# Optimization experiments

Measured on AMD Instinct MI355X. Metric: run time of the kernel, lower is better.

The kernel has to match this reference:

```python
import jax, jax.numpy as jnp
import numpy as np

B, HT_, WT_, DM, C = 32, 32, 32, 768, 64  # batch, token grid, token dim, hough channels
THETA_RES, RHO_RES = 3, 1


def hough_transform(rows, cols, theta_res, rho_res):
    """Precompute binary vote matrix [rows*cols, n_rho*n_theta] (HT-LCNN style)."""
    theta = np.linspace(0.0, 180.0, int(np.ceil(180.0 / theta_res)) + 1)[:-1]
    w = theta.size                                # n_theta
    diag = np.sqrt((rows - 1) ** 2 + (cols - 1) ** 2)
    q = int(np.ceil(diag / rho_res))
    nrho = 2 * q + 1                              # n_rho
    cos_t, sin_t = np.cos(np.deg2rad(theta)), np.sin(np.deg2rad(theta))
    ii, jj = np.meshgrid(np.arange(rows), np.arange(cols), indexing='ij')
    xc = jj - cols / 2.0                          # centered pixel coords
    yc = rows / 2.0 - ii
    rho = xc[..., None] * cos_t + yc[..., None] * sin_t   # [rows, cols, w]
    ridx = np.round(rho / rho_res).astype(np.int64) + q
    tidx = np.broadcast_to(np.arange(w), ridx.shape)
    flat = (ridx * w + tidx).reshape(rows * cols, w)      # bin = rho_idx*w + theta_idx
    vote = np.zeros((rows * cols, nrho * w), dtype=np.float32)
    vote[np.arange(rows * cols)[:, None], flat] = 1.0
    return vote, nrho, w


def setup_inputs() -> dict:
    key = jax.random.key(0)
    ks = jax.random.split(key, 8)
    vote_np, n_rho, n_theta = hough_transform(HT_, WT_, THETA_RES, RHO_RES)
    ch = C // 2
    s = lambda n: 1.0 / np.sqrt(n)
    return dict(
        tokens=jax.random.normal(ks[0], (B, HT_ * WT_, DM), jnp.float32),
        vote=jnp.asarray(vote_np),                                    # [N, HR]
        Wt_in=jax.random.normal(ks[1], (C, DM), jnp.float32) * s(DM),   # to_feats 1x1
        bt_in=jnp.zeros((C,), jnp.float32),
        W1=jax.random.normal(ks[2], (ch, C), jnp.float32) * s(C),       # conv1 1x1 (no bias)
        W2=jax.random.normal(ks[3], (ch, ch, 9, 1), jnp.float32) * s(ch * 9),  # (9,1) conv on hough map
        W3=jax.random.normal(ks[4], (C, ch), jnp.float32) * s(ch),      # conv3 1x1 (no bias)
        Wt_out=jax.random.normal(ks[5], (DM, C), jnp.float32) * s(C),   # from_feats 1x1
        bt_out=jnp.zeros((DM,), jnp.float32),
        n_rho=n_rho,
        n_theta=n_theta,
    )


def reference(tokens, vote, Wt_in, bt_in, W1, W2, W3, Wt_out, bt_out, n_rho, n_theta):
    # tokens: [B, N, D]; vote: [N, HR] with HR = n_rho * n_theta.
    # 1x1 convs over the token grid are position-independent -> plain matmuls on [B, N, *].
    norm = jnp.clip(vote.sum(0), 1.0)                       # [HR] HT vote-count normalizer
    feat = tokens @ Wt_in.T + bt_in                         # [B, N, C]   (to_feats)
    y = jax.nn.relu(feat @ W1.T)                            # [B, N, ch]  (conv1 + relu)
    # HT: relu (idempotent here) + vote gather as dense matmul, normalized per hough bin
    ht = jnp.einsum('bnc,nh->bch', y, vote) / norm          # [B, ch, HR]
    bb, ch, hr = ht.shape
    ht = ht.reshape(bb, ch, n_rho, n_theta)                 # [B, ch, n_rho, n_theta]
    ht = jax.lax.conv_general_dilated(                      # (9,1) conv along rho, pad 4
        ht, W2, (1, 1), ((4, 4), (0, 0)),
        dimension_numbers=('NCHW', 'OIHW', 'NCHW'))
    # IHT: relu + transposed vote scatter, normalized by n_theta
    iht = jnp.einsum('bch,nh->bnc', jax.nn.relu(ht.reshape(bb, ch, hr)), vote) / n_theta
    z = iht @ W3.T                                          # [B, N, C]   (conv3)
    out = (feat + z) @ Wt_out.T + bt_out                    # residual + from_feats -> [B, N, D]
    return out
```

## Files before the change

### kernel.cpp

```cpp
#include <hip/hip_runtime.h>
#include <math.h>

#define NB    32
#define NTOK  1024
#define DMODEL 768
#define CF    64
#define CHH   32
#define NRHO  89
#define NTH   60
#define HRB   (NRHO*NTH)

typedef short bf16x8 __attribute__((ext_vector_type(8)));
typedef float f32x4  __attribute__((ext_vector_type(4)));
typedef unsigned int uint;
typedef unsigned short ushort;
typedef unsigned char uchar;

__device__ __forceinline__ ushort f2bf(float f) {
    uint u = __float_as_uint(f);
    return (ushort)((u + 0x7FFF + ((u >> 16) & 1)) >> 16);
}
__device__ __forceinline__ float bf2f(ushort u) {
    return __uint_as_float(((uint)u) << 16);
}
__device__ __forceinline__ uint cvtpk(float lo, float hi) {
    uint r;
    asm("v_cvt_pk_bf16_f32 %0, %1, %2" : "=v"(r) : "v"(lo), "v"(hi));
    return r;
}

#define GLDS16(gp, lp) __builtin_amdgcn_global_load_lds( \
    (const __attribute__((address_space(1))) unsigned int*)(gp), \
    (__attribute__((address_space(3))) unsigned int*)(lp), 16, 0, 0)

__global__ __launch_bounds__(256) void k0_prep(
    int* __restrict__ perm, int* __restrict__ rowptr, uchar* __restrict__ rho8,
    const float* __restrict__ Wt_in, const float* __restrict__ bt_in,
    const float* __restrict__ W1, short* __restrict__ wcat,
    float* __restrict__ bcat,
    const float* __restrict__ Wt_out, const float* __restrict__ W2,
    short* __restrict__ wout, short* __restrict__ w2t) {
    __shared__ int rho_n[NTOK];
    __shared__ int cnt2[64 * 90];
    __shared__ int tot[96];
    __shared__ int base[96];
    __shared__ float w1row[64];
    const int tid = threadIdx.x;
    const int blk = blockIdx.x;

    if (blk < 60) {
        const int t = blk;
        const double rad = ((double)(t * 3)) * (M_PI / 180.0);
        const double ct = cos(rad), st = sin(rad);
        for (int n = tid; n < NTOK; n += 256) {
            int i = n >> 5, j = n & 31;
            double rho = (double)(j - 16) * ct + (double)(16 - i) * st;
            int ridx = (int)rint(rho) + 44;
            rho_n[n] = ridx;
            rho8[t * NTOK + n] = (uchar)ridx;
        }
        for (int i = tid; i < 64 * 90; i += 256) cnt2[i] = 0;
        __syncthreads();
        for (int n = tid; n < NTOK; n += 256)
            atomicAdd(&cnt2[(n >> 4) * 90 + rho_n[n]], 1);
        __syncthreads();
        if (tid < NRHO) {
            int s = 0;
            for (int c = 0; c < 64; ++c) {
                int v = cnt2[c * 90 + tid];
                cnt2[c * 90 + tid] = s;
                s += v;
            }
            tot[tid] = s;
        }
        __syncthreads();
        if (tid == 0) {
            int s = 0;
            for (int r = 0; r < NRHO; ++r) { base[r] = s; s += tot[r]; }
            base[NRHO] = s;
        }
        __syncthreads();
        if (tid < NRHO + 1) rowptr[t * 90 + tid] = base[tid];
        if (tid < 64) {
            const int c = tid;
            #pragma unroll
            for (int j = 0; j < 16; ++j) {
                int n = c * 16 + j;
                int r = rho_n[n];
                int cur = cnt2[c * 90 + r];
                cnt2[c * 90 + r] = cur + 1;
                perm[t * NTOK + base[r] + cur] = n;
            }
        }
    } else if (blk < 156) {
        const int c = blk - 60;
        if (c >= 64)
            for (int j = tid; j < 64; j += 256) w1row[j] = W1[(c - 64) * 64 + j];
        __syncthreads();
        for (int k = tid; k < DMODEL; k += 256) {
            float v;
            if (c < 64) v = Wt_in[c * DMODEL + k];
            else {
                v = 0.0f;
                for (int j = 0; j < 64; ++j) v += w1row[j] * Wt_in[j * DMODEL + k];
            }
            int kt = k >> 6, kk = k & 63;
            wcat[(((kt << 3) + (kk >> 3)) * 96 + c) * 8 + (k & 7)] = (short)f2bf(v);
        }
        if (tid == 0) {
            float bv;
            if (c < 64) bv = bt_in[c];
            else {
                bv = 0.0f;
                for (int j = 0; j < 64; ++j) bv += W1[(c - 64) * 64 + j] * bt_in[j];
            }
            bcat[c] = bv;
        }
    } else {
        int idx = (blk - 156) * 256 + tid;
        if (idx < 6144) {
            int d = idx >> 3, kg = idx & 7;
            float4 a = *(const float4*)&Wt_out[d * 64 + kg * 8];
            float4 b = *(const float4*)&Wt_out[d * 64 + kg * 8 + 4];
            uint4 v = make_uint4(cvtpk(a.x, a.y), cvtpk(a.z, a.w),
                                 cvtpk(b.x, b.y), cvtpk(b.z, b.w));
            *(uint4*)&wout[(((d >> 7) * 8 + kg) * 128 + (d & 127)) * 8] = v;
        } else if (idx < 6144 + 9216) {
            int q = idx - 6144;
            int e = q & 7, ln = (q >> 3) & 63, wm = (q >> 9) & 1, k = q >> 10;
            int o = wm * 16 + (ln & 15), i = ((ln >> 4) << 3) + e;
            w2t[q] = (short)f2bf(W2[(o * 32 + i) * 9 + k]);
        }
    }
}

__global__ __launch_bounds__(256) void k1_mfma(
    const float* __restrict__ tokens, const short* __restrict__ wcat,
    const float* __restrict__ bcat, ushort* __restrict__ featb,
    ushort* __restrict__ ybb) {
    __shared__ __align__(16) short Asm[2][4096];
    __shared__ __align__(16) short Bsm[2][6144];

    const int tid = threadIdx.x;
    const int lane = tid & 63, wave = tid >> 6;
    const int wm = wave >> 1, wn = wave & 1;
    const int row0 = blockIdx.x * 64;
    const int sm = tid >> 2, sq = tid & 3;

    const float* arow = tokens + (size_t)(row0 + sm) * DMODEL;

    f32x4 acc[2][3] = {};
    float4 ta[4];

    #pragma unroll
    for (int p = 0; p < 4; ++p)
        ta[p] = *(const float4*)&arow[(sq + 4 * p) * 4];
    for (int ch = tid; ch < 768; ch += 256)
        GLDS16((const char*)wcat + ch * 16, (char*)Bsm[0] + ch * 16);
    #pragma unroll
    for (int p = 0; p < 4; ++p) {
        int q = sq + 4 * p, kg = q >> 1, half = q & 1;
        uint lo = cvtpk(ta[p].x, ta[p].y);
        uint hi = cvtpk(ta[p].z, ta[p].w);
        *(uint2*)((char*)Asm[0] + (kg * 64 + sm) * 16 + half * 8) = make_uint2(lo, hi);
    }
    __syncthreads();

    int cur = 0;
    for (int kt = 0; kt < 12; ++kt) {
        if (kt < 11) {
            const float* src = arow + (kt + 1) * 64;
            #pragma unroll
            for (int p = 0; p < 4; ++p)
                ta[p] = *(const float4*)&src[(sq + 4 * p) * 4];
            const char* bsrc = (const char*)wcat + (size_t)(kt + 1) * 12288;
            for (int ch = tid; ch < 768; ch += 256)
                GLDS16(bsrc + ch * 16, (char*)Bsm[cur ^ 1] + ch * 16);
        }
        const bf16x8* Ap = (const bf16x8*)Asm[cur];
        const bf16x8* Bp = (const bf16x8*)Bsm[cur];
        #pragma unroll
        for (int ks = 0; ks < 2; ++ks) {
            int kg = (lane >> 4) + ks * 4;
            bf16x8 av[2], bv[3];
            #pragma unroll
            for (int i = 0; i < 2; ++i)
                av[i] = Ap[kg * 64 + wm * 32 + i * 16 + (lane & 15)];
            #pragma unroll
            for (int j = 0; j < 3; ++j)
                bv[j] = Bp[kg * 96 + wn * 48 + j * 16 + (lane & 15)];
            #pragma unroll
            for (int i = 0; i < 2; ++i)
                #pragma unroll
                for (int j = 0; j < 3; ++j)
                    acc[i][j] = __builtin_amdgcn_mfma_f32_16x16x32_bf16(
                        av[i], bv[j], acc[i][j], 0, 0, 0);
        }
        if (kt < 11) {
            #pragma unroll
            for (int p = 0; p < 4; ++p) {
                int q = sq + 4 * p, kg = q >> 1, half = q & 1;
                uint lo = cvtpk(ta[p].x, ta[p].y);
                uint hi = cvtpk(ta[p].z, ta[p].w);
                *(uint2*)((char*)Asm[cur ^ 1] + (kg * 64 + sm) * 16 + half * 8) =
                    make_uint2(lo, hi);
            }
        }
        __syncthreads();
        cur ^= 1;
    }

    ushort* fs = (ushort*)Asm[0];
    ushort* ys = (ushort*)Asm[1];
    float bb[3];
    #pragma unroll
    for (int j = 0; j < 3; ++j) bb[j] = bcat[wn * 48 + j * 16 + (lane & 15)];
    #pragma unroll
    for (int i = 0; i < 2; ++i) {
        #pragma unroll
        for (int j = 0; j < 3; ++j) {
            int c = wn * 48 + j * 16 + (lane & 15);
            int mlb = wm * 32 + i * 16 + ((lane >> 4) << 2);
            #pragma unroll
            for (int r = 0; r < 4; ++r) {
                float v = acc[i][j][r] + bb[j];
                if (c < 64) fs[(mlb + r) * 64 + c] = f2bf(v);
                else        ys[(mlb + r) * 32 + (c - 64)] = f2bf(fmaxf(v, 0.0f));
            }
        }
    }
    __syncthreads();
    for (int idx = tid; idx < 512; idx += 256) {
        int ml = idx >> 3, cq = (idx & 7) * 8;
        *(uint4*)&featb[(size_t)(row0 + ml) * CF + cq] = *(const uint4*)&fs[ml * 64 + cq];
    }
    {
        int ml = tid >> 2, cq = (tid & 3) * 8;
        *(uint4*)&ybb[(size_t)(row0 + ml) * CHH + cq] = *(const uint4*)&ys[ml * 32 + cq];
    }
}

__global__ __launch_bounds__(256) void k23_ht_conv(
    const ushort* __restrict__ ybb, const int* __restrict__ perm,
    const int* __restrict__ rowptr, const short* __restrict__ w2t,
    ushort* __restrict__ htcT) {
    __shared__ int pperm[NTOK];
    __shared__ int prow[90];
    __shared__ __align__(16) short insp[104 * 40];
    __shared__ uint outtu[NRHO * 18];

    const int tid = threadIdx.x;
    const int lane = tid & 63, wave = tid >> 6;
    const int wm = wave >> 1, wn = wave & 1;
    const int b = blockIdx.x / NTH, t = blockIdx.x % NTH;

    bf16x8 av[9];
    #pragma unroll
    for (int k = 0; k < 9; ++k)
        av[k] = *(const bf16x8*)&w2t[(((k * 2 + wm) * 64) + lane) * 8];

    for (int i = tid; i < NTOK; i += 256) pperm[i] = perm[t * NTOK + i];
    for (int i = tid; i < 90; i += 256) prow[i] = rowptr[t * 90 + i];
    for (int i = tid; i < 104 * 40 / 2; i += 256) ((uint*)insp)[i] = 0;
    __syncthreads();

    {
        const int c0 = (tid & 7) * 4, g = tid >> 3;
        const ushort* yp = ybb + (size_t)b * NTOK * CHH + c0;
        for (int rho = g; rho < NRHO; rho += 32) {
            int p0 = prow[rho], p1 = prow[rho + 1];
            float s0 = 0.0f, s1 = 0.0f, s2 = 0.0f, s3 = 0.0f;
            for (int k = p0; k < p1; ++k) {
                int n = pperm[k];
                ushort4 v = *(const ushort4*)&yp[n * CHH];
                s0 += bf2f(v.x); s1 += bf2f(v.y); s2 += bf2f(v.z); s3 += bf2f(v.w);
            }
            float iv = 1.0f / fmaxf((float)(p1 - p0), 1.0f);
            *(uint2*)&insp[(rho + 4) * 40 + c0] =
                make_uint2(cvtpk(s0 * iv, s1 * iv), cvtpk(s2 * iv, s3 * iv));
        }
    }
    __syncthreads();

    f32x4 acc[3] = {};
    #pragma unroll
    for (int f = 0; f < 3; ++f) {
        int Rn = wn * 48 + f * 16 + (lane & 15);
        #pragma unroll
        for (int k = 0; k < 9; ++k) {
            bf16x8 bv = *(const bf16x8*)&insp[(Rn + k) * 40 + ((lane >> 4) << 3)];
            acc[f] = __builtin_amdgcn_mfma_f32_16x16x32_bf16(av[k], bv, acc[f], 0, 0, 0);
        }
    }
    #pragma unroll
    for (int f = 0; f < 3; ++f) {
        int r = wn * 48 + f * 16 + (lane & 15);
        if (r < NRHO) {
            int ob = wm * 8 + ((lane >> 4) << 1);
            outtu[r * 18 + ob]     = cvtpk(fmaxf(acc[f][0], 0.0f), fmaxf(acc[f][1], 0.0f));
            outtu[r * 18 + ob + 1] = cvtpk(fmaxf(acc[f][2], 0.0f), fmaxf(acc[f][3], 0.0f));
        }
    }
    __syncthreads();

    {
        ushort* dst = htcT + (size_t)(b * NTH + t) * (NRHO * CHH);
        for (int idx = tid; idx < NRHO * 8; idx += 256) {
            int r = idx >> 3, q = idx & 7;
            uint2 v;
            v.x = outtu[r * 18 + q * 2];
            v.y = outtu[r * 18 + q * 2 + 1];
            *(uint2*)&dst[r * CHH + q * 4] = v;
        }
    }
}

__global__ __launch_bounds__(512) void k45_iht_out(
    const ushort* __restrict__ htcT, const uchar* __restrict__ rho8,
    const float* __restrict__ W3, const ushort* __restrict__ featb,
    const short* __restrict__ wout, const float* __restrict__ bt_out,
    float* __restrict__ out) {
    __shared__ __align__(16) char smem[81408];
    short* Alds = (short*)smem;
    short* Blds = (short*)(smem + 16384);
    float* w3t  = (float*)(smem + 49152);
    uchar* lrho = (uchar*)(smem + 57344);
    float* ihts = (float*)(smem + 65024);

    const int tid = threadIdx.x;
    const int lane = tid & 63, wave = tid >> 6;
    const int wm = wave >> 1, wn = wave & 1;
    const int b = blockIdx.x >> 3;
    const int n0 = (blockIdx.x & 7) * 128;

    for (int ch = tid; ch < 1024; ch += 512)
        GLDS16((const char*)wout + ch * 16, (char*)Blds + ch * 16);

    for (int idx = tid; idx < 2048; idx += 512) {
        int c = idx >> 6, j = idx & 63;
        w3t[idx] = W3[j * 32 + c];
    }
    for (int idx = tid; idx < NTH * 128; idx += 512)
        lrho[idx] = rho8[(idx >> 7) * NTOK + n0 + (idx & 127)];
    __syncthreads();

    {
        const int c0 = (tid & 3) * 8, tok = tid >> 2;
        const ushort* hb = htcT + (size_t)b * NTH * NRHO * CHH + c0;
        float s[8] = {};
        #pragma unroll 6
        for (int t = 0; t < NTH; ++t) {
            int r = lrho[t * 128 + tok];
            uint4 v = *(const uint4*)&hb[(size_t)(t * NRHO + r) * CHH];
            s[0] += bf2f((ushort)(v.x & 0xffff)); s[1] += bf2f((ushort)(v.x >> 16));
            s[2] += bf2f((ushort)(v.y & 0xffff)); s[3] += bf2f((ushort)(v.y >> 16));
            s[4] += bf2f((ushort)(v.z & 0xffff)); s[5] += bf2f((ushort)(v.z >> 16));
            s[6] += bf2f((ushort)(v.w & 0xffff)); s[7] += bf2f((ushort)(v.w >> 16));
        }
        float4 r0, r1;
        r0.x = s[0] * (1.0f / 60.0f); r0.y = s[1] * (1.0f / 60.0f);
        r0.z = s[2] * (1.0f / 60.0f); r0.w = s[3] * (1.0f / 60.0f);
        r1.x = s[4] * (1.0f / 60.0f); r1.y = s[5] * (1.0f / 60.0f);
        r1.z = s[6] * (1.0f / 60.0f); r1.w = s[7] * (1.0f / 60.0f);
        *(float4*)&ihts[tok * 32 + c0] = r0;
        *(float4*)&ihts[tok * 32 + c0 + 4] = r1;
    }
    __syncthreads();

    {
        const int j = tid & 63, nb = tid >> 6;
        ushort* Au = (ushort*)Alds;
        for (int nn = nb; nn < 128; nn += 8) {
            float z = 0.0f;
            #pragma unroll 8
            for (int cc = 0; cc < 32; ++cc) z += ihts[nn * 32 + cc] * w3t[cc * 64 + j];
            float v = bf2f(featb[((size_t)b * NTOK + n0 + nn) * CF + j]) + z;
            Au[((j >> 3) * 128 + nn) * 8 + (j & 7)] = f2bf(v);
        }
    }
    __syncthreads();

    const bf16x8* Ap = (const bf16x8*)Alds;
    for (int db = 0; db < 6; ++db) {
        if (db < 5) {
            const char* src = (const char*)wout + (size_t)(db + 1) * 16384;
            char* dst = (char*)Blds + ((db + 1) & 1) * 16384;
            for (int ch = tid; ch < 1024; ch += 512)
                GLDS16(src + ch * 16, dst + ch * 16);
        }
        const bf16x8* Bp = (const bf16x8*)((const char*)Blds + (db & 1) * 16384);
        f32x4 acc[2][4] = {};
        #pragma unroll
        for (int ks = 0; ks < 2; ++ks) {
            int kg = (lane >> 4) + ks * 4;
            bf16x8 avv[2], bvv[4];
            #pragma unroll
            for (int i = 0; i < 2; ++i)
                avv[i] = Ap[kg * 128 + wm * 32 + i * 16 + (lane & 15)];
            #pragma unroll
            for (int jf = 0; jf < 4; ++jf)
                bvv[jf] = Bp[kg * 128 + wn * 64 + jf * 16 + (lane & 15)];
            #pragma unroll
            for (int i = 0; i < 2; ++i)
                #pragma unroll
                for (int jf = 0; jf < 4; ++jf)
                    acc[i][jf] = __builtin_amdgcn_mfma_f32_16x16x32_bf16(
                        avv[i], bvv[jf], acc[i][jf], 0, 0, 0);
        }
        const int d0 = db * 128 + wn * 64 + (lane & 15);
        float bb[4];
        #pragma unroll
        for (int jf = 0; jf < 4; ++jf) bb[jf] = bt_out[d0 + jf * 16];
        const int mrow = blockIdx.x * 128 + wm * 32 + ((lane >> 4) << 2);
        #pragma unroll
        for (int i = 0; i < 2; ++i)
            #pragma unroll
            for (int r = 0; r < 4; ++r)
                #pragma unroll
                for (int jf = 0; jf < 4; ++jf)
                    out[(size_t)(mrow + i * 16 + r) * DMODEL + d0 + jf * 16] =
                        acc[i][jf][r] + bb[jf];
        __syncthreads();
    }
}

extern "C" void kernel_launch(void* const* d_in, const int* in_sizes, int n_in,
                              void* d_out, int out_size, void* d_ws, size_t ws_size,
                              hipStream_t stream) {
    const float* tokens = (const float*)d_in[0];
    const float* Wt_in  = (const float*)d_in[2];
    const float* bt_in  = (const float*)d_in[3];
    const float* W1     = (const float*)d_in[4];
    const float* W2     = (const float*)d_in[5];
    const float* W3     = (const float*)d_in[6];
    const float* Wt_out = (const float*)d_in[7];
    const float* bt_out = (const float*)d_in[8];
    float* out = (float*)d_out;

    char* w = (char*)d_ws;
    int*    perm   = (int*)(w);
    int*    rowptr = (int*)(w + 245760);
    uchar*  rho8   = (uchar*)(w + 267360);
    short*  wcat   = (short*)(w + 328800);
    float*  bcat   = (float*)(w + 476256);
    short*  wout   = (short*)(w + 476640);
    short*  w2t    = (short*)(w + 574944);
    ushort* featb  = (ushort*)(w + 593376);
    ushort* ybb    = (ushort*)(w + 4787680);
    ushort* htcT   = (ushort*)(w + 6884832);

    k0_prep<<<216, 256, 0, stream>>>(perm, rowptr, rho8, Wt_in, bt_in, W1,
                                     wcat, bcat, Wt_out, W2, wout, w2t);
    k1_mfma<<<NB * NTOK / 64, 256, 0, stream>>>(tokens, wcat, bcat, featb, ybb);
    k23_ht_conv<<<NB * NTH, 256, 0, stream>>>(ybb, perm, rowptr, w2t, htcT);
    k45_iht_out<<<NB * (NTOK / 128), 512, 0, stream>>>(htcT, rho8, W3, featb,
                                                       wout, bt_out, out);
}
```

Before: 101.0 us.

## Halve IHT/output tile, alias shared memory, and widen HT gather loads

The fused IHT plus output-projection kernel now handles 64 tokens per block with 256 threads instead of 128 tokens with 512. Shared memory is reused across phases: W3, rho and IHT scratch alias the B buffer, and the first weight tile is loaded only after those phases finish. Shared memory drops from about 81KB to 40KB, so more blocks can be resident and there are twice as many blocks. The cost is an extra sync and loading the first weight tile without overlap. In the HT gather, each thread now reads 8 channels per token with 16-byte loads instead of 4 channels with 8-byte loads.

```diff
diff --git a/kernel.cpp b/kernel.cpp
--- a/kernel.cpp
+++ b/kernel.cpp
@@ -265,19 +265,23 @@
     __syncthreads();
 
     {
-        const int c0 = (tid & 7) * 4, g = tid >> 3;
+        const int c0 = (tid & 3) * 8, g = tid >> 2;
         const ushort* yp = ybb + (size_t)b * NTOK * CHH + c0;
-        for (int rho = g; rho < NRHO; rho += 32) {
+        for (int rho = g; rho < NRHO; rho += 64) {
             int p0 = prow[rho], p1 = prow[rho + 1];
-            float s0 = 0.0f, s1 = 0.0f, s2 = 0.0f, s3 = 0.0f;
+            float s0 = 0, s1 = 0, s2 = 0, s3 = 0, s4 = 0, s5 = 0, s6 = 0, s7 = 0;
             for (int k = p0; k < p1; ++k) {
                 int n = pperm[k];
-                ushort4 v = *(const ushort4*)&yp[n * CHH];
-                s0 += bf2f(v.x); s1 += bf2f(v.y); s2 += bf2f(v.z); s3 += bf2f(v.w);
+                uint4 v = *(const uint4*)&yp[n * CHH];
+                s0 += bf2f((ushort)(v.x & 0xffff)); s1 += bf2f((ushort)(v.x >> 16));
+                s2 += bf2f((ushort)(v.y & 0xffff)); s3 += bf2f((ushort)(v.y >> 16));
+                s4 += bf2f((ushort)(v.z & 0xffff)); s5 += bf2f((ushort)(v.z >> 16));
+                s6 += bf2f((ushort)(v.w & 0xffff)); s7 += bf2f((ushort)(v.w >> 16));
             }
             float iv = 1.0f / fmaxf((float)(p1 - p0), 1.0f);
-            *(uint2*)&insp[(rho + 4) * 40 + c0] =
-                make_uint2(cvtpk(s0 * iv, s1 * iv), cvtpk(s2 * iv, s3 * iv));
+            uint4 pk = make_uint4(cvtpk(s0 * iv, s1 * iv), cvtpk(s2 * iv, s3 * iv),
+                                  cvtpk(s4 * iv, s5 * iv), cvtpk(s6 * iv, s7 * iv));
+            *(uint4*)&insp[(rho + 4) * 40 + c0] = pk;
         }
     }
     __syncthreads();
@@ -315,33 +319,31 @@
     }
 }
 
-__global__ __launch_bounds__(512) void k45_iht_out(
+__global__ __launch_bounds__(256, 4) void k45_iht_out(
     const ushort* __restrict__ htcT, const uchar* __restrict__ rho8,
     const float* __restrict__ W3, const ushort* __restrict__ featb,
     const short* __restrict__ wout, const float* __restrict__ bt_out,
     float* __restrict__ out) {
-    __shared__ __align__(16) char smem[81408];
-    short* Alds = (short*)smem;
-    short* Blds = (short*)(smem + 16384);
-    float* w3t  = (float*)(smem + 49152);
-    uchar* lrho = (uchar*)(smem + 57344);
-    float* ihts = (float*)(smem + 65024);
+    __shared__ __align__(16) char smem[40960];
+    short* Blds = (short*)smem;
+    short* Alds = (short*)(smem + 32768);
+    float* w3t  = (float*)smem;
+    uchar* lrho = (uchar*)(smem + 8192);
+    float* ihts = (float*)(smem + 12032);
 
     const int tid = threadIdx.x;
     const int lane = tid & 63, wave = tid >> 6;
     const int wm = wave >> 1, wn = wave & 1;
-    const int b = blockIdx.x >> 3;
-    const int n0 = (blockIdx.x & 7) * 128;
-
-    for (int ch = tid; ch < 1024; ch += 512)
-        GLDS16((const char*)wout + ch * 16, (char*)Blds + ch * 16);
-
-    for (int idx = tid; idx < 2048; idx += 512) {
+    const int bid = blockIdx.x;
+    const int b = bid >> 4;
+    const int n0 = (bid & 15) * 64;
+
+    for (int idx = tid; idx < 2048; idx += 256) {
         int c = idx >> 6, j = idx & 63;
         w3t[idx] = W3[j * 32 + c];
     }
-    for (int idx = tid; idx < NTH * 128; idx += 512)
-        lrho[idx] = rho8[(idx >> 7) * NTOK + n0 + (idx & 127)];
+    for (int idx = tid; idx < NTH * 64; idx += 256)
+        lrho[idx] = rho8[(idx >> 6) * NTOK + n0 + (idx & 63)];
     __syncthreads();
 
     {
@@ -350,13 +352,14 @@
         float s[8] = {};
         #pragma unroll 6
         for (int t = 0; t < NTH; ++t) {
-            int r = lrho[t * 128 + tok];
+            int r = lrho[t * 64 + tok];
             uint4 v = *(const uint4*)&hb[(size_t)(t * NRHO + r) * CHH];
             s[0] += bf2f((ushort)(v.x & 0xffff)); s[1] += bf2f((ushort)(v.x >> 16));
             s[2] += bf2f((ushort)(v.y & 0xffff)); s[3] += bf2f((ushort)(v.y >> 16));
             s[4] += bf2f((ushort)(v.z & 0xffff)); s[5] += bf2f((ushort)(v.z >> 16));
             s[6] += bf2f((ushort)(v.w & 0xffff)); s[7] += bf2f((ushort)(v.w >> 16));
         }
+        __syncthreads();
         float4 r0, r1;
         r0.x = s[0] * (1.0f / 60.0f); r0.y = s[1] * (1.0f / 60.0f);
         r0.z = s[2] * (1.0f / 60.0f); r0.w = s[3] * (1.0f / 60.0f);
@@ -370,14 +373,18 @@
     {
         const int j = tid & 63, nb = tid >> 6;
         ushort* Au = (ushort*)Alds;
-        for (int nn = nb; nn < 128; nn += 8) {
+        for (int nn = nb; nn < 64; nn += 4) {
             float z = 0.0f;
             #pragma unroll 8
             for (int cc = 0; cc < 32; ++cc) z += ihts[nn * 32 + cc] * w3t[cc * 64 + j];
-            float v = bf2f(featb[((size_t)b * NTOK + n0 + nn) * CF + j]) + z;
-            Au[((j >> 3) * 128 + nn) * 8 + (j & 7)] = f2bf(v);
-        }
-    }
+            float v = bf2f(featb[(size_t)(bid * 64 + nn) * CF + j]) + z;
+            Au[((j >> 3) * 64 + nn) * 8 + (j & 7)] = f2bf(v);
+        }
+    }
+    __syncthreads();
+
+    for (int ch = tid; ch < 1024; ch += 256)
+        GLDS16((const char*)wout + ch * 16, (char*)Blds + ch * 16);
     __syncthreads();
 
     const bf16x8* Ap = (const bf16x8*)Alds;
@@ -385,7 +392,7 @@
         if (db < 5) {
             const char* src = (const char*)wout + (size_t)(db + 1) * 16384;
             char* dst = (char*)Blds + ((db + 1) & 1) * 16384;
-            for (int ch = tid; ch < 1024; ch += 512)
+            for (int ch = tid; ch < 1024; ch += 256)
                 GLDS16(src + ch * 16, dst + ch * 16);
         }
         const bf16x8* Bp = (const bf16x8*)((const char*)Blds + (db & 1) * 16384);
@@ -396,7 +403,7 @@
             bf16x8 avv[2], bvv[4];
             #pragma unroll
             for (int i = 0; i < 2; ++i)
-                avv[i] = Ap[kg * 128 + wm * 32 + i * 16 + (lane & 15)];
+                avv[i] = Ap[kg * 64 + wm * 32 + i * 16 + (lane & 15)];
             #pragma unroll
             for (int jf = 0; jf < 4; ++jf)
                 bvv[jf] = Bp[kg * 128 + wn * 64 + jf * 16 + (lane & 15)];
@@ -411,7 +418,7 @@
         float bb[4];
         #pragma unroll
         for (int jf = 0; jf < 4; ++jf) bb[jf] = bt_out[d0 + jf * 16];
-        const int mrow = blockIdx.x * 128 + wm * 32 + ((lane >> 4) << 2);
+        const int mrow = bid * 64 + wm * 32 + ((lane >> 4) << 2);
         #pragma unroll
         for (int i = 0; i < 2; ++i)
             #pragma unroll
@@ -453,6 +460,6 @@
                                      wcat, bcat, Wt_out, W2, wout, w2t);
     k1_mfma<<<NB * NTOK / 64, 256, 0, stream>>>(tokens, wcat, bcat, featb, ybb);
     k23_ht_conv<<<NB * NTH, 256, 0, stream>>>(ybb, perm, rowptr, w2t, htcT);
-    k45_iht_out<<<NB * (NTOK / 128), 512, 0, stream>>>(htcT, rho8, W3, featb,
-                                                       wout, bt_out, out);
-}
+    k45_iht_out<<<NB * (NTOK / 64), 256, 0, stream>>>(htcT, rho8, W3, featb,
+                                                      wout, bt_out, out);
+}
```

New measurement: 100.4 us. About the same (-0.6%).
